# Performance work log

Hardware: AMD Instinct MI355X
Metric: run time of the kernel (lower is better)

Reference implementation:

```python
import jax, jax.numpy as jnp
import numpy as np

INT_STEPS = 7
SHAPE = (1, 3, 160, 192, 224)  # [B, 3, D, H, W]


def _grid_sample_3d(vol, coords):
    """Trilinear 3D grid_sample, padding_mode='zeros', align_corners=True.

    vol:    [B, C, D, H, W]
    coords: [B, 3, D, H, W] sample positions in VOXEL space (d, h, w order).
    Note: torch normalizes to [-1,1] then grid_sample (align_corners=True)
    maps back to [0, size-1]; the two cancel, so we sample in voxel coords.
    """
    B, C, D, H, W = vol.shape
    N = D * H * W
    volf = vol.reshape(B, C, N)
    d, h, w = coords[:, 0], coords[:, 1], coords[:, 2]  # each [B, D, H, W]
    d0 = jnp.floor(d)
    h0 = jnp.floor(h)
    w0 = jnp.floor(w)
    fd, fh, fw = d - d0, h - h0, w - w0
    d0i = d0.astype(jnp.int32)
    h0i = h0.astype(jnp.int32)
    w0i = w0.astype(jnp.int32)
    out = jnp.zeros_like(vol)
    # 8 trilinear corners; out-of-bounds corners contribute 0 (zeros padding).
    for cd, wd in ((d0i, 1.0 - fd), (d0i + 1, fd)):
        for chh, wh in ((h0i, 1.0 - fh), (h0i + 1, fh)):
            for cw, ww in ((w0i, 1.0 - fw), (w0i + 1, fw)):
                valid = (cd >= 0) & (cd < D) & (chh >= 0) & (chh < H) & (cw >= 0) & (cw < W)
                idx = (jnp.clip(cd, 0, D - 1) * H + jnp.clip(chh, 0, H - 1)) * W + jnp.clip(cw, 0, W - 1)
                vals = jnp.take_along_axis(volf, idx.reshape(B, 1, N), axis=2).reshape(B, C, D, H, W)
                wgt = (wd * wh * ww * valid.astype(vol.dtype))[:, None]  # [B,1,D,H,W]
                out = out + vals * wgt
    return out


def setup_inputs() -> dict:
    key = jax.random.key(0)
    SVF = jax.random.normal(key, SHAPE, dtype=jnp.float32)
    return {"SVF": SVF}


def reference(SVF) -> jnp.ndarray:
    B, C, D, H, W = SVF.shape
    gd, gh, gw = jnp.meshgrid(jnp.arange(D), jnp.arange(H), jnp.arange(W), indexing="ij")
    grid = jnp.stack([gd, gh, gw])[None].astype(SVF.dtype)  # [1, 3, D, H, W]
    flow = SVF * (1.0 / 2.0 ** INT_STEPS)
    for _ in range(INT_STEPS):  # scaling and squaring
        new_locs = grid + flow  # voxel-space sample positions
        flow = flow + _grid_sample_3d(flow, new_locs)
    return flow
```

## Files before the change

### kernel.cpp

```cpp
#include <hip/hip_runtime.h>
#include <hip/hip_fp16.h>


#define D_ 160
#define H_ 192
#define W_ 224
static constexpr int NV = D_ * H_ * W_;
static constexpr int HW = H_ * W_;
static constexpr float S_ = 0.0078125f;
typedef unsigned int u32;

struct __attribute__((packed, aligned(8))) U4 { u32 a, b, c, d; };
struct __attribute__((packed, aligned(8))) U2 { u32 a, b; };

__device__ __forceinline__ float2 h2f(u32 h) {
    __half2 x = *(__half2*)&h;
    return __half22float2(x);
}
__device__ __forceinline__ u32 pk(float a, float b) {
    __half2 h = __floats2half2_rn(a, b);
    return *(u32*)&h;
}
__device__ __forceinline__ float h1f(u32 bits16) {
    __half_raw r; r.x = (unsigned short)bits16;
    return __half2float(__half(r));
}

__global__ __launch_bounds__(256) void scale_k(const float* __restrict__ svf,
                                               u32* __restrict__ out) {
    const int i = blockIdx.x * 256 + threadIdx.x;
    float4 a = ((const float4*)svf)[i];
    float4 b = ((const float4*)(svf + NV))[i];
    float4 c = ((const float4*)(svf + 2 * NV))[i];
    u32* o = out + 8 * (size_t)i;
    o[0] = pk(a.x * S_, b.x * S_);  o[1] = pk(c.x * S_, 0.f);
    o[2] = pk(a.y * S_, b.y * S_);  o[3] = pk(c.y * S_, 0.f);
    o[4] = pk(a.z * S_, b.z * S_);  o[5] = pk(c.z * S_, 0.f);
    o[6] = pk(a.w * S_, b.w * S_);  o[7] = pk(c.w * S_, 0.f);
}

__device__ __forceinline__ void lerp_windows(const U4& u0, const U4& u1,
                                             const U4& u2, const U4& u3,
                                             float fd, float fh, float fw,
                                             float& a0, float& a1, float& a2) {
    const float ww1 = fw, ww0 = 1.f - fw;
    const float wh1 = fh, wh0 = 1.f - fh;
    const float wd1 = fd, wd0 = 1.f - fd;
    const float c00 = wd0 * wh0, c01 = wd0 * wh1;
    const float c10 = wd1 * wh0, c11 = wd1 * wh1;
    {
        const float2 q0 = h2f(u0.a), q1 = h2f(u0.c);
        const float z0 = h1f(u0.b & 0xffffu), z1 = h1f(u0.d & 0xffffu);
        a0 = c00 * (ww0 * q0.x + ww1 * q1.x);
        a1 = c00 * (ww0 * q0.y + ww1 * q1.y);
        a2 = c00 * (ww0 * z0 + ww1 * z1);
    }
    {
        const float2 q0 = h2f(u1.a), q1 = h2f(u1.c);
        const float z0 = h1f(u1.b & 0xffffu), z1 = h1f(u1.d & 0xffffu);
        a0 += c01 * (ww0 * q0.x + ww1 * q1.x);
        a1 += c01 * (ww0 * q0.y + ww1 * q1.y);
        a2 += c01 * (ww0 * z0 + ww1 * z1);
    }
    {
        const float2 q0 = h2f(u2.a), q1 = h2f(u2.c);
        const float z0 = h1f(u2.b & 0xffffu), z1 = h1f(u2.d & 0xffffu);
        a0 += c10 * (ww0 * q0.x + ww1 * q1.x);
        a1 += c10 * (ww0 * q0.y + ww1 * q1.y);
        a2 += c10 * (ww0 * z0 + ww1 * z1);
    }
    {
        const float2 q0 = h2f(u3.a), q1 = h2f(u3.c);
        const float z0 = h1f(u3.b & 0xffffu), z1 = h1f(u3.d & 0xffffu);
        a0 += c11 * (ww0 * q0.x + ww1 * q1.x);
        a1 += c11 * (ww0 * q0.y + ww1 * q1.y);
        a2 += c11 * (ww0 * z0 + ww1 * z1);
    }
}

__device__ __forceinline__ void lerp_general(const u32* __restrict__ in,
                                             int d0, int h0, int w0,
                                             float fd, float fh, float fw,
                                             float& a0, float& a1, float& a2) {
    a0 = a1 = a2 = 0.f;
    const __half* hp = (const __half*)in;
#pragma unroll
    for (int dz = 0; dz < 2; ++dz) {
        const int cd = d0 + dz;
        if ((unsigned)cd >= (unsigned)D_) continue;
        const float wz = dz ? fd : (1.f - fd);
#pragma unroll
        for (int dy = 0; dy < 2; ++dy) {
            const int ch = h0 + dy;
            if ((unsigned)ch >= (unsigned)H_) continue;
            const float wzy = wz * (dy ? fh : (1.f - fh));
            const int rowbase = (cd * H_ + ch) * W_;
#pragma unroll
            for (int dx = 0; dx < 2; ++dx) {
                const int cw = w0 + dx;
                if ((unsigned)cw >= (unsigned)W_) continue;
                const float wt = wzy * (dx ? fw : (1.f - fw));
                const int j = 4 * (rowbase + cw);
                a0 += wt * __half2float(hp[j]);
                a1 += wt * __half2float(hp[j + 1]);
                a2 += wt * __half2float(hp[j + 2]);
            }
        }
    }
}

template <int PLANAR_OUT>
__global__ __launch_bounds__(256) void compose_k(const u32* __restrict__ in,
                                                 void* __restrict__ out_) {
    const int w = blockIdx.x * 32 + threadIdx.x;
    const int h = blockIdx.y * 4 + threadIdx.y;
    const int d = (blockIdx.z * 2 + threadIdx.z) * 2;
    const int idx0 = (d * H_ + h) * W_ + w;
    const int idx1 = idx0 + HW;

    const U2 uoA = *(const U2*)(in + 2 * (size_t)idx0);
    const U2 uoB = *(const U2*)(in + 2 * (size_t)idx1);

    const float2 fA01 = h2f(uoA.a);
    const float fA0 = fA01.x, fA1 = fA01.y, fA2 = h1f(uoA.b & 0xffffu);
    const float2 fB01 = h2f(uoB.a);
    const float fB0 = fB01.x, fB1 = fB01.y, fB2 = h1f(uoB.b & 0xffffu);

    const float pdA = (float)d + fA0,       phA = (float)h + fA1, pwA = (float)w + fA2;
    const float pdB = (float)(d + 1) + fB0, phB = (float)h + fB1, pwB = (float)w + fB2;

    const float dAf = floorf(pdA), hAf = floorf(phA), wAf = floorf(pwA);
    const float dBf = floorf(pdB), hBf = floorf(phB), wBf = floorf(pwB);
    const int d0A = (int)dAf, h0A = (int)hAf, w0A = (int)wAf;
    const int d0B = (int)dBf, h0B = (int)hBf, w0B = (int)wBf;
    const float fdA = pdA - dAf, fhA = phA - hAf, fwA = pwA - wAf;
    const float fdB = pdB - dBf, fhB = phB - hBf, fwB = pwB - wBf;

    const bool intA = ((unsigned)d0A <= (unsigned)(D_ - 2)) &
                      ((unsigned)h0A <= (unsigned)(H_ - 2)) &
                      ((unsigned)w0A <= (unsigned)(W_ - 2));
    const bool intB = ((unsigned)d0B <= (unsigned)(D_ - 2)) &
                      ((unsigned)h0B <= (unsigned)(H_ - 2)) &
                      ((unsigned)w0B <= (unsigned)(W_ - 2));

    float aA0, aA1, aA2, aB0, aB1, aB2;

    if (intA & intB) {
        const int jA = (d0A * H_ + h0A) * W_ + w0A;
        const int jB = (d0B * H_ + h0B) * W_ + w0B;
        const U4 uA0 = *(const U4*)(in + 2 * (size_t)jA);
        const U4 uA1 = *(const U4*)(in + 2 * (size_t)(jA + W_));
        const U4 uA2 = *(const U4*)(in + 2 * (size_t)(jA + HW));
        const U4 uA3 = *(const U4*)(in + 2 * (size_t)(jA + HW + W_));
        const U4 uB0 = *(const U4*)(in + 2 * (size_t)jB);
        const U4 uB1 = *(const U4*)(in + 2 * (size_t)(jB + W_));
        const U4 uB2 = *(const U4*)(in + 2 * (size_t)(jB + HW));
        const U4 uB3 = *(const U4*)(in + 2 * (size_t)(jB + HW + W_));

        lerp_windows(uA0, uA1, uA2, uA3, fdA, fhA, fwA, aA0, aA1, aA2);
        lerp_windows(uB0, uB1, uB2, uB3, fdB, fhB, fwB, aB0, aB1, aB2);
    } else {
        lerp_general(in, d0A, h0A, w0A, fdA, fhA, fwA, aA0, aA1, aA2);
        lerp_general(in, d0B, h0B, w0B, fdB, fhB, fwB, aB0, aB1, aB2);
    }

    const float oA0 = fA0 + aA0, oA1 = fA1 + aA1, oA2 = fA2 + aA2;
    const float oB0 = fB0 + aB0, oB1 = fB1 + aB1, oB2 = fB2 + aB2;

    if (PLANAR_OUT) {
        float* out = (float*)out_;
        out[idx0] = oA0; out[NV + idx0] = oA1; out[2 * NV + idx0] = oA2;
        out[idx1] = oB0; out[NV + idx1] = oB1; out[2 * NV + idx1] = oB2;
    } else {
        U2 oA; oA.a = pk(oA0, oA1); oA.b = pk(oA2, 0.f);
        U2 oB; oB.a = pk(oB0, oB1); oB.b = pk(oB2, 0.f);
        *(U2*)((u32*)out_ + 2 * (size_t)idx0) = oA;
        *(U2*)((u32*)out_ + 2 * (size_t)idx1) = oB;
    }
}

extern "C" void kernel_launch(void* const* d_in, const int* in_sizes, int n_in,
                              void* d_out, int out_size, void* d_ws, size_t ws_size,
                              hipStream_t stream) {
    const float* svf = (const float*)d_in[0];
    float* outp = (float*)d_out;
    u32* X0 = (u32*)d_ws;
    u32* X1 = (u32*)d_out;

    scale_k<<<NV / 4 / 256, 256, 0, stream>>>(svf, X0);

    dim3 blk(32, 4, 2);
    dim3 grd(W_ / 32, H_ / 4, D_ / 4);

    compose_k<0><<<grd, blk, 0, stream>>>(X0, X1);
    compose_k<0><<<grd, blk, 0, stream>>>(X1, X0);
    compose_k<0><<<grd, blk, 0, stream>>>(X0, X1);
    compose_k<0><<<grd, blk, 0, stream>>>(X1, X0);
    compose_k<0><<<grd, blk, 0, stream>>>(X0, X1);
    compose_k<0><<<grd, blk, 0, stream>>>(X1, X0);
    compose_k<1><<<grd, blk, 0, stream>>>(X0, outp);
}
```

Measured before the change: 324.9 us.

## Pair adjacent-W voxels per thread and swizzle workgroups across XCDs

Each thread now handles two voxels adjacent along W rather than along D, so the own-flow read and the output write become single 16-byte accesses, and the planar output uses float2 stores. The block tile changes to 32w×8h×2d. A 1D grid is remapped so that contiguous spatial tiles go to the same XCD (bid&7 selects the chunk), improving L2 locality for the gathers. The risks are a different gather footprint per block and extra integer division work for the index decode.

```diff
diff --git a/kernel.cpp b/kernel.cpp
--- a/kernel.cpp
+++ b/kernel.cpp
@@ -10,8 +10,11 @@
 static constexpr float S_ = 0.0078125f;
 typedef unsigned int u32;
 
+static constexpr int NWG   = 13440;
+static constexpr int PERX  = NWG / 8;
+static constexpr int PERD2 = 7 * 24;
+
 struct __attribute__((packed, aligned(8))) U4 { u32 a, b, c, d; };
-struct __attribute__((packed, aligned(8))) U2 { u32 a, b; };
 
 __device__ __forceinline__ float2 h2f(u32 h) {
     __half2 x = *(__half2*)&h;
@@ -112,22 +115,26 @@
 template <int PLANAR_OUT>
 __global__ __launch_bounds__(256) void compose_k(const u32* __restrict__ in,
                                                  void* __restrict__ out_) {
-    const int w = blockIdx.x * 32 + threadIdx.x;
-    const int h = blockIdx.y * 4 + threadIdx.y;
-    const int d = (blockIdx.z * 2 + threadIdx.z) * 2;
+    const int bid = blockIdx.x;
+    const int wk  = (bid & 7) * PERX + (bid >> 3);
+    const int db2 = wk / PERD2;
+    const int rem = wk - db2 * PERD2;
+    const int hb  = rem / 7;
+    const int wb  = rem - hb * 7;
+
+    const int w = wb * 32 + 2 * threadIdx.x;
+    const int h = hb * 8 + threadIdx.y;
+    const int d = db2 * 2 + threadIdx.z;
     const int idx0 = (d * H_ + h) * W_ + w;
-    const int idx1 = idx0 + HW;
-
-    const U2 uoA = *(const U2*)(in + 2 * (size_t)idx0);
-    const U2 uoB = *(const U2*)(in + 2 * (size_t)idx1);
-
-    const float2 fA01 = h2f(uoA.a);
-    const float fA0 = fA01.x, fA1 = fA01.y, fA2 = h1f(uoA.b & 0xffffu);
-    const float2 fB01 = h2f(uoB.a);
-    const float fB0 = fB01.x, fB1 = fB01.y, fB2 = h1f(uoB.b & 0xffffu);
-
-    const float pdA = (float)d + fA0,       phA = (float)h + fA1, pwA = (float)w + fA2;
-    const float pdB = (float)(d + 1) + fB0, phB = (float)h + fB1, pwB = (float)w + fB2;
+
+    const U4 uo = *(const U4*)(in + 2 * (size_t)idx0);
+    const float2 fA01 = h2f(uo.a);
+    const float fA0 = fA01.x, fA1 = fA01.y, fA2 = h1f(uo.b & 0xffffu);
+    const float2 fB01 = h2f(uo.c);
+    const float fB0 = fB01.x, fB1 = fB01.y, fB2 = h1f(uo.d & 0xffffu);
+
+    const float pdA = (float)d + fA0, phA = (float)h + fA1, pwA = (float)w + fA2;
+    const float pdB = (float)d + fB0, phB = (float)h + fB1, pwB = (float)(w + 1) + fB2;
 
     const float dAf = floorf(pdA), hAf = floorf(phA), wAf = floorf(pwA);
     const float dBf = floorf(pdB), hBf = floorf(phB), wBf = floorf(pwB);
@@ -169,13 +176,14 @@
 
     if (PLANAR_OUT) {
         float* out = (float*)out_;
-        out[idx0] = oA0; out[NV + idx0] = oA1; out[2 * NV + idx0] = oA2;
-        out[idx1] = oB0; out[NV + idx1] = oB1; out[2 * NV + idx1] = oB2;
+        *(float2*)(out + idx0)          = make_float2(oA0, oB0);
+        *(float2*)(out + NV + idx0)     = make_float2(oA1, oB1);
+        *(float2*)(out + 2 * NV + idx0) = make_float2(oA2, oB2);
     } else {
-        U2 oA; oA.a = pk(oA0, oA1); oA.b = pk(oA2, 0.f);
-        U2 oB; oB.a = pk(oB0, oB1); oB.b = pk(oB2, 0.f);
-        *(U2*)((u32*)out_ + 2 * (size_t)idx0) = oA;
-        *(U2*)((u32*)out_ + 2 * (size_t)idx1) = oB;
+        U4 o;
+        o.a = pk(oA0, oA1); o.b = pk(oA2, 0.f);
+        o.c = pk(oB0, oB1); o.d = pk(oB2, 0.f);
+        *(U4*)((u32*)out_ + 2 * (size_t)idx0) = o;
     }
 }
 
@@ -189,8 +197,8 @@
 
     scale_k<<<NV / 4 / 256, 256, 0, stream>>>(svf, X0);
 
-    dim3 blk(32, 4, 2);
-    dim3 grd(W_ / 32, H_ / 4, D_ / 4);
+    dim3 blk(16, 8, 2);
+    dim3 grd(NWG, 1, 1);
 
     compose_k<0><<<grd, blk, 0, stream>>>(X0, X1);
     compose_k<0><<<grd, blk, 0, stream>>>(X1, X0);
```

Result: faster. 297.2 us (-8.5%).
